# Kernel tuning notes

Hardware: AMD Instinct MI355X
Metric: run time of the kernel (lower is better)

Reference implementation:

```python
import jax, jax.numpy as jnp
import numpy as np
from jax import lax

EPS = 1e-5

def binarize(x):
    # sign forward, straight-through (identity) backward, matching torch .data-trick Binarize
    return x + lax.stop_gradient(jnp.sign(x) - x)

def conv2d(x, w, pad):
    return lax.conv_general_dilated(x, w, window_strides=(1, 1),
                                    padding=[(pad, pad), (pad, pad)],
                                    dimension_numbers=('NCHW', 'OIHW', 'NCHW'))

def maxpool_k2s1(x):
    return lax.reduce_window(x, -jnp.inf, lax.max, (1, 1, 2, 2), (1, 1, 1, 1), 'VALID')

def batchnorm(x, g, b):
    # training-mode BN: batch statistics over (N, H, W)
    mean = jnp.mean(x, axis=(0, 2, 3), keepdims=True)
    var = jnp.var(x, axis=(0, 2, 3), keepdims=True)
    return (x - mean) * lax.rsqrt(var + EPS) * g[None, :, None, None] + b[None, :, None, None]

def hardtanh(x):
    return jnp.clip(x, -1.0, 1.0)

def setup_inputs() -> dict:
    key = jax.random.key(0)
    ks = jax.random.split(key, 11)
    B = 4096
    return {
        'x':   jax.random.normal(ks[0], (B, 12, 12, 15), jnp.float32),
        'w1':  jax.random.normal(ks[1], (48, 12, 3, 3), jnp.float32) * 0.1,
        'g1':  1.0 + 0.1 * jax.random.normal(ks[2], (48,), jnp.float32),
        'b1':  0.1 * jax.random.normal(ks[3], (48,), jnp.float32),
        'w2':  jax.random.normal(ks[4], (48, 48, 3, 3), jnp.float32) * 0.1,
        'g2':  1.0 + 0.1 * jax.random.normal(ks[5], (48,), jnp.float32),
        'b2':  0.1 * jax.random.normal(ks[6], (48,), jnp.float32),
        'w3':  jax.random.normal(ks[7], (48, 48, 3, 3), jnp.float32) * 0.1,
        'g3':  1.0 + 0.1 * jax.random.normal(ks[8], (48,), jnp.float32),
        'b3':  0.1 * jax.random.normal(ks[9], (48,), jnp.float32),
        'wfc': jax.random.normal(ks[10], (5, 54 * 48), jnp.float32) * 0.02,
    }

def reference(x, w1, g1, b1, w2, g2, b2, w3, g3, b3, wfc):
    # BinarizeConv2d binarizes activations (in_channels != 3) and weights; returns binarized input too
    xb1 = binarize(x)                                  # [B,12,12,15]
    h = conv2d(xb1, binarize(w1), pad=1)               # [B,48,12,15]
    h = maxpool_k2s1(h)                                # [B,48,11,14]
    h = hardtanh(batchnorm(h, g1, b1))
    xb2 = binarize(h)
    h = conv2d(xb2, binarize(w2), pad=0)               # [B,48,9,12]
    h = hardtanh(batchnorm(h, g2, b2))
    xb3 = binarize(h)
    h = conv2d(xb3, binarize(w3), pad=0)               # [B,48,7,10]
    h = maxpool_k2s1(h)                                # [B,48,6,9] -> 54 spatial
    h = hardtanh(batchnorm(h, g3, b3))
    f = h.reshape(h.shape[0], -1)                      # [B, 2592]
    fb = binarize(f)
    out = fb @ binarize(wfc).T                         # [B, 5]  (LogSoftmax defined but never applied)
    return (out, xb1, xb2, xb3, fb)
```

## Files before the change

kernel.cpp:

```cpp
#include <hip/hip_runtime.h>
#include <stdint.h>

typedef unsigned long long u64;
typedef unsigned int u32;
typedef unsigned short u16;
typedef unsigned char u8;
typedef signed char s8;

#define NB 4096

#define WS_STATS 0
#define WS_W1Q   20480
#define WS_W2P   24576
#define WS_W3P   28672
#define WS_WFCP  32768
#define WS_A2    40960
#define WS_P1    5087232
#define WS_P3    5087232

#define OUT_OFF 0
#define XB1_OFF 20480
#define XB2_OFF 8867840
#define XB3_OFF 39145472
#define FB_OFF  60379136

__device__ __forceinline__ float fsign(float v) {
    return (v > 0.0f) ? 1.0f : ((v < 0.0f) ? -1.0f : 0.0f);
}
__device__ __forceinline__ int sh16(int v, int h) {
    return h ? (v >> 16) : (int)(short)v;
}

__global__ __launch_bounds__(512)
void kw_pack(const float* __restrict__ w1, const float* __restrict__ w2,
             const float* __restrict__ w3, const float* __restrict__ wfc,
             u32* __restrict__ W1Q, u64* __restrict__ W2P, u64* __restrict__ W3P,
             u64* __restrict__ WFCP, long long* __restrict__ stats) {
    int t = threadIdx.x;
    for (int i = t; i < 2304; i += 512) stats[i] = 0;
    if (t < 48) {
        u16 m1[9];
        #pragma unroll
        for (int p = 0; p < 9; ++p) {
            u16 m = 0;
            for (int c = 0; c < 12; ++c)
                if (w1[t*108 + c*9 + p] > 0.0f) m |= (u16)(1u << c);
            m1[p] = m;
        }
        #pragma unroll
        for (int j = 0; j < 4; ++j)
            W1Q[t*5 + j] = (u32)m1[2*j] | ((u32)m1[2*j+1] << 16);
        W1Q[t*5 + 4] = (u32)m1[8];
    }
    if (t < 432) {
        int oc = t / 9, p = t % 9;
        u64 m2 = 0, m3 = 0;
        for (int c = 0; c < 48; ++c) {
            if (w2[oc*432 + c*9 + p] > 0.0f) m2 |= (1ull << c);
            if (w3[oc*432 + c*9 + p] > 0.0f) m3 |= (1ull << c);
        }
        W2P[t] = m2;
        W3P[t] = m3;
    }
    if (t < 205) {
        int o = t / 41, j = t % 41;
        u64 m = 0;
        for (int l = 0; l < 64; ++l) {
            int k = j*64 + l;
            if (k < 2592 && wfc[o*2592 + k] > 0.0f) m |= (1ull << l);
        }
        WFCP[t] = m;
    }
}

__global__ __launch_bounds__(192)
void k1(const float* __restrict__ x, const u32* __restrict__ W1Q,
        float* __restrict__ dout, u8* __restrict__ P1g, u64* __restrict__ stats) {
    __shared__ u8 bitsb[2160];
    __shared__ u16 As[180];
    __shared__ int cmap[2304];
    __shared__ int2 part[192];
    int t = threadIdx.x, b = blockIdx.x;
    {
        const float4* xp = (const float4*)(x + (size_t)b*2160);
        float4* xo = (float4*)(dout + XB1_OFF + (size_t)b*2160);
        for (int j = t; j < 540; j += 192) {
            float4 v = xp[j];
            float4 o;
            o.x = fsign(v.x); o.y = fsign(v.y); o.z = fsign(v.z); o.w = fsign(v.w);
            xo[j] = o;
            bitsb[4*j]   = v.x > 0.0f;
            bitsb[4*j+1] = v.y > 0.0f;
            bitsb[4*j+2] = v.z > 0.0f;
            bitsb[4*j+3] = v.w > 0.0f;
        }
    }
    __syncthreads();
    if (t < 180) {
        u16 m = 0;
        #pragma unroll
        for (int c = 0; c < 12; ++c)
            m |= ((u16)bitsb[c*180 + t]) << c;
        As[t] = m;
    }
    __syncthreads();
    if (t < 180) {
        int y = t / 15, xx = t % 15;
        u16 tap[9], msk[9];
        int nv = 0;
        #pragma unroll
        for (int ky = 0; ky < 3; ++ky) {
            #pragma unroll
            for (int kx = 0; kx < 3; ++kx) {
                int yy = y + ky - 1, xc = xx + kx - 1;
                bool v = (yy >= 0 && yy < 12 && xc >= 0 && xc < 15);
                int yl = min(max(yy, 0), 11), xl = min(max(xc, 0), 14);
                tap[ky*3+kx] = As[yl*15 + xl];
                msk[ky*3+kx] = v ? (u16)0xFFFF : (u16)0;
                nv += v ? 12 : 0;
            }
        }
        u32 tq[5], mq[5];
        #pragma unroll
        for (int j = 0; j < 4; ++j) {
            tq[j] = (u32)tap[2*j] | ((u32)tap[2*j+1] << 16);
            mq[j] = (u32)msk[2*j] | ((u32)msk[2*j+1] << 16);
        }
        tq[4] = tap[8]; mq[4] = msk[8];
        s8* cb = (s8*)cmap;
        #pragma unroll 4
        for (int oc = 0; oc < 48; ++oc) {
            int acc = 0;
            #pragma unroll
            for (int j = 0; j < 5; ++j)
                acc += __popc((tq[j] ^ W1Q[oc*5 + j]) & mq[j]);
            cb[oc*192 + y*16 + xx] = (s8)(nv - 2*acc);
        }
    }
    __syncthreads();
    {
        int c = t >> 2, q = t & 3;
        int r0 = 3*q, nr = (q < 3) ? 3 : 2;
        int rowv[4][4];
        #pragma unroll
        for (int j = 0; j < 4; ++j)
            if (j <= nr) {
                #pragma unroll
                for (int i = 0; i < 4; ++i)
                    rowv[j][i] = cmap[c*48 + (r0 + j)*4 + i];
            }
        int sum = 0, sq = 0;
        u8* gp = P1g + (size_t)b*8448 + c*176;
        #pragma unroll
        for (int pr = 0; pr < 3; ++pr) {
            if (pr < nr) {
                int o0 = 0, o1 = 0, o2 = 0, o3 = 0;
                #pragma unroll
                for (int k = 0; k < 14; ++k) {
                    int a0 = (int)(s8)(rowv[pr][k>>2] >> (8*(k&3)));
                    int a1 = (int)(s8)(rowv[pr][(k+1)>>2] >> (8*((k+1)&3)));
                    int b0 = (int)(s8)(rowv[pr+1][k>>2] >> (8*(k&3)));
                    int b1 = (int)(s8)(rowv[pr+1][(k+1)>>2] >> (8*((k+1)&3)));
                    int mx = max(max(a0, a1), max(b0, b1));
                    sum += mx; sq += mx*mx;
                    int shl = 8*(k&3);
                    if ((k>>2) == 0) o0 |= (mx & 255) << shl;
                    else if ((k>>2) == 1) o1 |= (mx & 255) << shl;
                    else if ((k>>2) == 2) o2 |= (mx & 255) << shl;
                    else o3 |= (mx & 255) << shl;
                }
                *((int4*)(gp + (r0 + pr)*16)) = make_int4(o0, o1, o2, o3);
            }
        }
        part[t] = make_int2(sum, sq);
    }
    __syncthreads();
    if (t < 48) {
        int s = 0, q = 0;
        #pragma unroll
        for (int k = 0; k < 4; ++k) { s += part[t*4+k].x; q += part[t*4+k].y; }
        int slot = b & 7;
        atomicAdd(&stats[t*8 + slot],        (u64)(long long)s);
        atomicAdd(&stats[(48 + t)*8 + slot], (u64)(long long)q);
    }
}

__global__ __launch_bounds__(256)
void kA(const float* __restrict__ g1, const float* __restrict__ b1,
        const long long* __restrict__ statsIn, const u8* __restrict__ P1g,
        u64* __restrict__ A2, const u64* __restrict__ W2,
        u64* __restrict__ statsOut) {
    __shared__ float sc[48], sh[48];
    __shared__ u64 As[154];
    __shared__ short c2s[5184];
    __shared__ int2 part[192];
    int t = threadIdx.x, b = blockIdx.x;
    if (t < 48) {
        long long s = 0, q = 0;
        #pragma unroll
        for (int k = 0; k < 8; ++k) { s += statsIn[t*8 + k]; q += statsIn[(48 + t)*8 + k]; }
        double N = 630784.0;
        double mean = (double)s / N;
        double var  = (double)q / N - mean*mean;
        double scale = (double)g1[t] / sqrt(var + 1e-5);
        sc[t] = (float)scale;
        sh[t] = (float)((double)b1[t] - mean*scale);
    }
    __syncthreads();
    if (t < 154) {
        int row = t / 14, px = t - 14*row;
        const u8* pb = P1g + (size_t)b*8448 + row*16 + px;
        u64 m = 0;
        #pragma unroll
        for (int c = 0; c < 48; ++c)
            if (sc[c]*(float)(s8)pb[c*176] + sh[c] > 0.0f) m |= (1ull << c);
        As[t] = m;
        A2[(size_t)b*154 + t] = m;
    }
    __syncthreads();
    if (t < 216) {
        int pos = (t < 108) ? t : (t - 108);
        int ocb = (t < 108) ? 0 : 24;
        int oy = pos / 12, ox = pos - 12*oy;
        u64 tap[9];
        #pragma unroll
        for (int ky = 0; ky < 3; ++ky)
            #pragma unroll
            for (int kx = 0; kx < 3; ++kx)
                tap[ky*3+kx] = As[(oy+ky)*14 + ox + kx];
        #pragma unroll 4
        for (int oc = ocb; oc < ocb + 24; ++oc) {
            int acc = 0;
            #pragma unroll
            for (int k = 0; k < 9; ++k)
                acc += __popcll(tap[k] ^ W2[oc*9 + k]);
            c2s[oc*108 + pos] = (short)(432 - 2*acc);
        }
    }
    __syncthreads();
    if (t < 192) {
        int c = t >> 2, q = t & 3;
        const int* ci = (const int*)(c2s + c*108);
        int sum = 0, sq = 0;
        for (int j = q; j < 54; j += 4) {
            int v2 = ci[j];
            int lo = (int)(short)v2, hi = v2 >> 16;
            sum += lo + hi; sq += lo*lo + hi*hi;
        }
        part[t] = make_int2(sum, sq);
    }
    __syncthreads();
    if (t < 48) {
        int s = 0, q = 0;
        #pragma unroll
        for (int k = 0; k < 4; ++k) { s += part[t*4+k].x; q += part[t*4+k].y; }
        int slot = b & 7;
        atomicAdd(&statsOut[(96 + t)*8 + slot],  (u64)(long long)s);
        atomicAdd(&statsOut[(144 + t)*8 + slot], (u64)(long long)q);
    }
}

__global__ __launch_bounds__(256)
void kS2(const float* __restrict__ g1, const float* __restrict__ b1,
         const long long* __restrict__ statsIn, const u8* __restrict__ P1g,
         float* __restrict__ dout) {
    __shared__ float sc[48], sh[48];
    int t = threadIdx.x;
    if (t < 48) {
        long long s = 0, q = 0;
        #pragma unroll
        for (int k = 0; k < 8; ++k) { s += statsIn[t*8 + k]; q += statsIn[(48 + t)*8 + k]; }
        double N = 630784.0;
        double mean = (double)s / N;
        double var  = (double)q / N - mean*mean;
        double scale = (double)g1[t] / sqrt(var + 1e-5);
        sc[t] = (float)scale;
        sh[t] = (float)((double)b1[t] - mean*scale);
    }
    __syncthreads();
    float4* xo = (float4*)(dout + XB2_OFF);
    int gid = blockIdx.x*256 + t;
    for (int j = gid; j < 7569408; j += 1048576) {
        int base = 4*j;
        int b = base / 7392;
        int u = base - 7392*b;
        const u8* pb = P1g + (size_t)b*8448;
        float r[4];
        #pragma unroll
        for (int k = 0; k < 4; ++k) {
            int uk = u + k;
            int c = uk / 154;
            int s = uk - 154*c;
            int row = s / 14;
            int px = s - 14*row;
            int v = (int)(s8)pb[c*176 + row*16 + px];
            r[k] = fsign(sc[c]*(float)v + sh[c]);
        }
        float4 o; o.x = r[0]; o.y = r[1]; o.z = r[2]; o.w = r[3];
        xo[j] = o;
    }
}

__global__ __launch_bounds__(256)
void kB(const float* __restrict__ g2, const float* __restrict__ b2,
        const long long* __restrict__ statsIn, const u64* __restrict__ A2,
        const u64* __restrict__ W2, const u64* __restrict__ W3,
        float* __restrict__ dout, int* __restrict__ P3i,
        u64* __restrict__ statsOut) {
    __shared__ float sc[48], sh[48];
    __shared__ u64 As[154];
    __shared__ short c2s[5184];
    __shared__ u64 A3[108];
    __shared__ short cm[3360];
    __shared__ int2 part[192];
    int t = threadIdx.x, b = blockIdx.x;
    if (t < 154) As[t] = A2[(size_t)b*154 + t];
    if (t < 48) {
        long long s = 0, q = 0;
        #pragma unroll
        for (int k = 0; k < 8; ++k) { s += statsIn[(96 + t)*8 + k]; q += statsIn[(144 + t)*8 + k]; }
        double N = 442368.0;
        double mean = (double)s / N;
        double var  = (double)q / N - mean*mean;
        double scale = (double)g2[t] / sqrt(var + 1e-5);
        sc[t] = (float)scale;
        sh[t] = (float)((double)b2[t] - mean*scale);
    }
    __syncthreads();
    if (t < 216) {
        int pos = (t < 108) ? t : (t - 108);
        int ocb = (t < 108) ? 0 : 24;
        int oy = pos / 12, ox = pos - 12*oy;
        u64 tap[9];
        #pragma unroll
        for (int ky = 0; ky < 3; ++ky)
            #pragma unroll
            for (int kx = 0; kx < 3; ++kx)
                tap[ky*3+kx] = As[(oy+ky)*14 + ox + kx];
        #pragma unroll 4
        for (int oc = ocb; oc < ocb + 24; ++oc) {
            int acc = 0;
            #pragma unroll
            for (int k = 0; k < 9; ++k)
                acc += __popcll(tap[k] ^ W2[oc*9 + k]);
            c2s[oc*108 + pos] = (short)(432 - 2*acc);
        }
    }
    __syncthreads();
    float4* xo = (float4*)(dout + XB3_OFF + (size_t)b*5184);
    for (int i4 = t; i4 < 1296; i4 += 256) {
        int c = i4 / 27, s4 = i4 - 27*c;
        short4 v4 = *(const short4*)&c2s[c*108 + s4*4];
        float4 o;
        o.x = fsign(sc[c]*(float)v4.x + sh[c]);
        o.y = fsign(sc[c]*(float)v4.y + sh[c]);
        o.z = fsign(sc[c]*(float)v4.z + sh[c]);
        o.w = fsign(sc[c]*(float)v4.w + sh[c]);
        xo[i4] = o;
    }
    if (t < 108) {
        u64 m = 0;
        #pragma unroll
        for (int c = 0; c < 48; ++c)
            if (sc[c]*(float)c2s[c*108 + t] + sh[c] > 0.0f) m |= (1ull << c);
        A3[t] = m;
    }
    __syncthreads();
    if (t < 210) {
        int grp = (t < 70) ? 0 : ((t < 140) ? 1 : 2);
        int pos = t - grp*70;
        int ocb = grp*16;
        int oy = pos / 10, ox = pos - 10*oy;
        u64 tap[9];
        #pragma unroll
        for (int ky = 0; ky < 3; ++ky)
            #pragma unroll
            for (int kx = 0; kx < 3; ++kx)
                tap[ky*3+kx] = A3[(oy+ky)*12 + ox + kx];
        #pragma unroll 4
        for (int oc = ocb; oc < ocb + 16; ++oc) {
            int acc = 0;
            #pragma unroll
            for (int k = 0; k < 9; ++k)
                acc += __popcll(tap[k] ^ W3[oc*9 + k]);
            cm[oc*70 + pos] = (short)(432 - 2*acc);
        }
    }
    __syncthreads();
    {
        int c = t >> 2, q = t & 3;
        if (t < 192) {
            int pr0 = (q < 2) ? 2*q : (q + 2);
            int npr = (q < 2) ? 2 : 1;
            int rowv[3][5];
            const int* cmi = (const int*)(cm + c*70);
            #pragma unroll
            for (int j = 0; j < 3; ++j)
                if (j <= npr) {
                    #pragma unroll
                    for (int i = 0; i < 5; ++i)
                        rowv[j][i] = cmi[(pr0 + j)*5 + i];
                }
            int sum = 0, sq = 0;
            int* gp = P3i + (size_t)b*1440 + c*30;
            #pragma unroll
            for (int pr = 0; pr < 2; ++pr) {
                if (pr < npr) {
                    int o[5] = {0, 0, 0, 0, 0};
                    #pragma unroll
                    for (int k = 0; k < 9; ++k) {
                        int a0 = sh16(rowv[pr][k>>1], k&1);
                        int a1 = sh16(rowv[pr][(k+1)>>1], (k+1)&1);
                        int b0 = sh16(rowv[pr+1][k>>1], k&1);
                        int b1 = sh16(rowv[pr+1][(k+1)>>1], (k+1)&1);
                        int mx = max(max(a0, a1), max(b0, b1));
                        sum += mx; sq += mx*mx;
                        o[k>>1] |= (mx & 0xffff) << (16*(k&1));
                    }
                    #pragma unroll
                    for (int j = 0; j < 5; ++j) gp[(pr0 + pr)*5 + j] = o[j];
                }
            }
            part[t] = make_int2(sum, sq);
        }
    }
    __syncthreads();
    if (t < 48) {
        int s = 0, q = 0;
        #pragma unroll
        for (int k = 0; k < 4; ++k) { s += part[t*4+k].x; q += part[t*4+k].y; }
        int slot = b & 7;
        atomicAdd(&statsOut[(192 + t)*8 + slot], (u64)(long long)s);
        atomicAdd(&statsOut[(240 + t)*8 + slot], (u64)(long long)q);
    }
}

__global__ __launch_bounds__(256)
void kC(const float* __restrict__ g3, const float* __restrict__ b3,
        const long long* __restrict__ statsIn, const int4* __restrict__ P3g4,
        const u64* __restrict__ WFC, float* __restrict__ dout) {
    __shared__ float sc[48], sh[48];
    __shared__ int smP[1440];
    __shared__ u8 nib[648];
    __shared__ u64 fbb[41];
    int t = threadIdx.x, b = blockIdx.x;
    for (int i = t; i < 360; i += 256) ((int4*)smP)[i] = P3g4[(size_t)b*360 + i];
    if (t < 48) {
        long long s = 0, q = 0;
        #pragma unroll
        for (int k = 0; k < 8; ++k) { s += statsIn[(192 + t)*8 + k]; q += statsIn[(240 + t)*8 + k]; }
        double N = 221184.0;
        double mean = (double)s / N;
        double var  = (double)q / N - mean*mean;
        double scale = (double)g3[t] / sqrt(var + 1e-5);
        sc[t] = (float)scale;
        sh[t] = (float)((double)b3[t] - mean*scale);
    }
    __syncthreads();
    const short* smS = (const short*)smP;
    float4* fo = (float4*)(dout + FB_OFF + (size_t)b*2592);
    for (int i4 = t; i4 < 648; i4 += 256) {
        int i = 4*i4;
        float r[4];
        unsigned n = 0;
        #pragma unroll
        for (int k = 0; k < 4; ++k) {
            int idx = i + k;
            int c = idx / 54, s = idx - 54*c;
            int row = s / 9, px = s - 9*row;
            float bn = sc[c]*(float)smS[c*60 + row*10 + px] + sh[c];
            r[k] = fsign(bn);
            if (bn > 0.0f) n |= (1u << k);
        }
        float4 o; o.x = r[0]; o.y = r[1]; o.z = r[2]; o.w = r[3];
        fo[i4] = o;
        nib[i4] = (u8)n;
    }
    __syncthreads();
    if (t < 41) {
        u64 m = 0;
        #pragma unroll
        for (int k = 0; k < 16; ++k) {
            int j = t*16 + k;
            if (j < 648) m |= ((u64)nib[j]) << (4*k);
        }
        fbb[t] = m;
    }
    __syncthreads();
    if (t < 5) {
        const u64* Wf = WFC + t*41;
        int acc = 0;
        #pragma unroll
        for (int j = 0; j < 41; ++j) acc += __popcll(fbb[j] ^ Wf[j]);
        dout[OUT_OFF + b*5 + t] = (float)(2592 - 2*acc);
    }
}

extern "C" void kernel_launch(void* const* d_in, const int* in_sizes, int n_in,
                              void* d_out, int out_size, void* d_ws, size_t ws_size,
                              hipStream_t stream) {
    const float* x   = (const float*)d_in[0];
    const float* w1  = (const float*)d_in[1];
    const float* g1  = (const float*)d_in[2];
    const float* b1  = (const float*)d_in[3];
    const float* w2  = (const float*)d_in[4];
    const float* g2  = (const float*)d_in[5];
    const float* b2  = (const float*)d_in[6];
    const float* w3  = (const float*)d_in[7];
    const float* g3  = (const float*)d_in[8];
    const float* b3  = (const float*)d_in[9];
    const float* wfc = (const float*)d_in[10];
    float* out = (float*)d_out;
    char* ws = (char*)d_ws;

    long long* stats = (long long*)(ws + WS_STATS);
    u32*       W1Q   = (u32*)(ws + WS_W1Q);
    u64*       W2P   = (u64*)(ws + WS_W2P);
    u64*       W3P   = (u64*)(ws + WS_W3P);
    u64*       WFCP  = (u64*)(ws + WS_WFCP);
    u64*       A2    = (u64*)(ws + WS_A2);
    u8*        P1g   = (u8*)(ws + WS_P1);
    int*       P3i   = (int*)(ws + WS_P3);

    hipLaunchKernelGGL(kw_pack, dim3(1),    dim3(512), 0, stream,
                       w1, w2, w3, wfc, W1Q, W2P, W3P, WFCP, stats);
    hipLaunchKernelGGL(k1,      dim3(NB),   dim3(192), 0, stream,
                       x, W1Q, out, P1g, (u64*)stats);
    hipLaunchKernelGGL(kA,      dim3(NB),   dim3(256), 0, stream,
                       g1, b1, stats, P1g, A2, W2P, (u64*)stats);
    hipLaunchKernelGGL(kS2,     dim3(NB),   dim3(256), 0, stream,
                       g1, b1, stats, P1g, out);
    hipLaunchKernelGGL(kB,      dim3(NB),   dim3(256), 0, stream,
                       g2, b2, stats, A2, W2P, W3P, out, P3i, (u64*)stats);
    hipLaunchKernelGGL(kC,      dim3(NB),   dim3(256), 0, stream,
                       g3, b3, stats, (const int4*)P3i, WFCP, out);
}
```

Measured before the change: 641.9 us.

## Split fused per-image BNN pipeline into many flat element-parallel kernels

Replaces the per-image fused kernels kA, kB and kC with a chain of small flat kernels. These finalize the BN constants once, pack activations, run conv2 without recomputing it, reduce per-channel stats, and handle conv3 with fused maxpool, the fb output and an FC step done by wavefront ballot. Conv2 was previously computed twice (once in kA for stats and again in kB); it is now computed once and stored channel-major in global memory. The cost is extra global round trips for the intermediate tensors, more kernel launches, and single-block-per-channel stat reductions with only 48 blocks, which limits parallelism.

```diff
diff --git a/kernel.cpp b/kernel.cpp
--- a/kernel.cpp
+++ b/kernel.cpp
@@ -10,13 +10,17 @@
 #define NB 4096
 
 #define WS_STATS 0
+#define WS_CST   18432
 #define WS_W1Q   20480
 #define WS_W2P   24576
 #define WS_W3P   28672
 #define WS_WFCP  32768
 #define WS_A2    40960
 #define WS_P1    5087232
-#define WS_P3    5087232
+#define WS_C2T   5087232
+#define WS_P3T   5087232
+#define WS_P3B   26320896
+#define WS_A3    40960
 
 #define OUT_OFF 0
 #define XB1_OFF 20480
@@ -70,6 +74,23 @@
             if (k < 2592 && wfc[o*2592 + k] > 0.0f) m |= (1ull << l);
         }
         WFCP[t] = m;
+    }
+}
+
+__global__ __launch_bounds__(64)
+void kbn(const float* __restrict__ g, const float* __restrict__ bb,
+         const long long* __restrict__ st, float* __restrict__ cst, float Nf) {
+    int t = threadIdx.x;
+    if (t < 48) {
+        long long s = 0, q = 0;
+        #pragma unroll
+        for (int k = 0; k < 8; ++k) { s += st[t*8 + k]; q += st[(48 + t)*8 + k]; }
+        double N = (double)Nf;
+        double mean = (double)s / N;
+        double var  = (double)q / N - mean*mean;
+        double scale = (double)g[t] / sqrt(var + 1e-5);
+        cst[t]      = (float)scale;
+        cst[48 + t] = (float)((double)bb[t] - mean*scale);
     }
 }
 
@@ -186,97 +207,31 @@
 }
 
 __global__ __launch_bounds__(256)
-void kA(const float* __restrict__ g1, const float* __restrict__ b1,
-        const long long* __restrict__ statsIn, const u8* __restrict__ P1g,
-        u64* __restrict__ A2, const u64* __restrict__ W2,
-        u64* __restrict__ statsOut) {
+void kM2(const float* __restrict__ cst, const u8* __restrict__ P1g,
+         u64* __restrict__ A2) {
     __shared__ float sc[48], sh[48];
-    __shared__ u64 As[154];
-    __shared__ short c2s[5184];
-    __shared__ int2 part[192];
-    int t = threadIdx.x, b = blockIdx.x;
-    if (t < 48) {
-        long long s = 0, q = 0;
-        #pragma unroll
-        for (int k = 0; k < 8; ++k) { s += statsIn[t*8 + k]; q += statsIn[(48 + t)*8 + k]; }
-        double N = 630784.0;
-        double mean = (double)s / N;
-        double var  = (double)q / N - mean*mean;
-        double scale = (double)g1[t] / sqrt(var + 1e-5);
-        sc[t] = (float)scale;
-        sh[t] = (float)((double)b1[t] - mean*scale);
-    }
-    __syncthreads();
-    if (t < 154) {
-        int row = t / 14, px = t - 14*row;
-        const u8* pb = P1g + (size_t)b*8448 + row*16 + px;
-        u64 m = 0;
-        #pragma unroll
-        for (int c = 0; c < 48; ++c)
-            if (sc[c]*(float)(s8)pb[c*176] + sh[c] > 0.0f) m |= (1ull << c);
-        As[t] = m;
-        A2[(size_t)b*154 + t] = m;
-    }
-    __syncthreads();
-    if (t < 216) {
-        int pos = (t < 108) ? t : (t - 108);
-        int ocb = (t < 108) ? 0 : 24;
-        int oy = pos / 12, ox = pos - 12*oy;
-        u64 tap[9];
-        #pragma unroll
-        for (int ky = 0; ky < 3; ++ky)
-            #pragma unroll
-            for (int kx = 0; kx < 3; ++kx)
-                tap[ky*3+kx] = As[(oy+ky)*14 + ox + kx];
-        #pragma unroll 4
-        for (int oc = ocb; oc < ocb + 24; ++oc) {
-            int acc = 0;
-            #pragma unroll
-            for (int k = 0; k < 9; ++k)
-                acc += __popcll(tap[k] ^ W2[oc*9 + k]);
-            c2s[oc*108 + pos] = (short)(432 - 2*acc);
-        }
-    }
-    __syncthreads();
-    if (t < 192) {
-        int c = t >> 2, q = t & 3;
-        const int* ci = (const int*)(c2s + c*108);
-        int sum = 0, sq = 0;
-        for (int j = q; j < 54; j += 4) {
-            int v2 = ci[j];
-            int lo = (int)(short)v2, hi = v2 >> 16;
-            sum += lo + hi; sq += lo*lo + hi*hi;
-        }
-        part[t] = make_int2(sum, sq);
-    }
-    __syncthreads();
-    if (t < 48) {
-        int s = 0, q = 0;
-        #pragma unroll
-        for (int k = 0; k < 4; ++k) { s += part[t*4+k].x; q += part[t*4+k].y; }
-        int slot = b & 7;
-        atomicAdd(&statsOut[(96 + t)*8 + slot],  (u64)(long long)s);
-        atomicAdd(&statsOut[(144 + t)*8 + slot], (u64)(long long)q);
-    }
-}
-
-__global__ __launch_bounds__(256)
-void kS2(const float* __restrict__ g1, const float* __restrict__ b1,
-         const long long* __restrict__ statsIn, const u8* __restrict__ P1g,
+    int t = threadIdx.x;
+    if (t < 48) sc[t] = cst[t];
+    else if (t < 96) sh[t-48] = cst[t];
+    __syncthreads();
+    int g = blockIdx.x*256 + t;
+    int b = g / 154, s = g - 154*b;
+    int row = s / 14, px = s - 14*row;
+    const u8* pb = P1g + (size_t)b*8448 + row*16 + px;
+    u64 m = 0;
+    #pragma unroll
+    for (int c = 0; c < 48; ++c)
+        if (sc[c]*(float)(s8)pb[c*176] + sh[c] > 0.0f) m |= (1ull << c);
+    A2[g] = m;
+}
+
+__global__ __launch_bounds__(256)
+void kS2(const float* __restrict__ cst, const u8* __restrict__ P1g,
          float* __restrict__ dout) {
     __shared__ float sc[48], sh[48];
     int t = threadIdx.x;
-    if (t < 48) {
-        long long s = 0, q = 0;
-        #pragma unroll
-        for (int k = 0; k < 8; ++k) { s += statsIn[t*8 + k]; q += statsIn[(48 + t)*8 + k]; }
-        double N = 630784.0;
-        double mean = (double)s / N;
-        double var  = (double)q / N - mean*mean;
-        double scale = (double)g1[t] / sqrt(var + 1e-5);
-        sc[t] = (float)scale;
-        sh[t] = (float)((double)b1[t] - mean*scale);
-    }
+    if (t < 48) sc[t] = cst[t];
+    else if (t < 96) sh[t-48] = cst[t];
     __syncthreads();
     float4* xo = (float4*)(dout + XB2_OFF);
     int gid = blockIdx.x*256 + t;
@@ -302,197 +257,211 @@
 }
 
 __global__ __launch_bounds__(256)
-void kB(const float* __restrict__ g2, const float* __restrict__ b2,
-        const long long* __restrict__ statsIn, const u64* __restrict__ A2,
-        const u64* __restrict__ W2, const u64* __restrict__ W3,
-        float* __restrict__ dout, int* __restrict__ P3i,
-        u64* __restrict__ statsOut) {
+void kCv2(const u64* __restrict__ A2, const u64* __restrict__ W2,
+          short* __restrict__ C2T) {
+    __shared__ u64 W2s[432];
+    int t = threadIdx.x;
+    for (int i = t; i < 432; i += 256) W2s[i] = W2[i];
+    __syncthreads();
+    int g = blockIdx.x*256 + t;
+    int b = g / 108, s = g - 108*b;
+    int oy = s / 12, ox = s - 12*oy;
+    const u64* ab = A2 + (size_t)b*154;
+    u64 tap[9];
+    #pragma unroll
+    for (int ky = 0; ky < 3; ++ky)
+        #pragma unroll
+        for (int kx = 0; kx < 3; ++kx)
+            tap[ky*3+kx] = ab[(oy+ky)*14 + ox + kx];
+    #pragma unroll 4
+    for (int oc = 0; oc < 48; ++oc) {
+        int acc = 0;
+        #pragma unroll
+        for (int k = 0; k < 9; ++k)
+            acc += __popcll(tap[k] ^ W2s[oc*9 + k]);
+        C2T[(size_t)oc*442368 + b*108 + s] = (short)(432 - 2*acc);
+    }
+}
+
+__global__ __launch_bounds__(256)
+void kSt(const short* __restrict__ src, int perChan,
+         long long* __restrict__ stats, int base) {
+    __shared__ long long redS[4], redQ[4];
+    int t = threadIdx.x, c = blockIdx.x;
+    const int* p = (const int*)(src + (size_t)c*perChan);
+    int n2 = perChan >> 1;
+    int sum = 0, sq = 0;
+    for (int j = t; j < n2; j += 256) {
+        int v2 = p[j];
+        int lo = (int)(short)v2, hi = v2 >> 16;
+        sum += lo + hi; sq += lo*lo + hi*hi;
+    }
+    long long ls = sum, lq = sq;
+    #pragma unroll
+    for (int off = 32; off >= 1; off >>= 1) {
+        ls += __shfl_down(ls, off);
+        lq += __shfl_down(lq, off);
+    }
+    int wv = t >> 6, ln = t & 63;
+    if (ln == 0) { redS[wv] = ls; redQ[wv] = lq; }
+    __syncthreads();
+    if (t == 0) {
+        long long S = redS[0]+redS[1]+redS[2]+redS[3];
+        long long Q = redQ[0]+redQ[1]+redQ[2]+redQ[3];
+        stats[(base + c)*8]      = S;
+        stats[(base + 48 + c)*8] = Q;
+    }
+}
+
+__global__ __launch_bounds__(256)
+void kX3(const float* __restrict__ cst, const short* __restrict__ C2T,
+         float* __restrict__ dout) {
     __shared__ float sc[48], sh[48];
-    __shared__ u64 As[154];
-    __shared__ short c2s[5184];
-    __shared__ u64 A3[108];
-    __shared__ short cm[3360];
-    __shared__ int2 part[192];
-    int t = threadIdx.x, b = blockIdx.x;
-    if (t < 154) As[t] = A2[(size_t)b*154 + t];
-    if (t < 48) {
-        long long s = 0, q = 0;
-        #pragma unroll
-        for (int k = 0; k < 8; ++k) { s += statsIn[(96 + t)*8 + k]; q += statsIn[(144 + t)*8 + k]; }
-        double N = 442368.0;
-        double mean = (double)s / N;
-        double var  = (double)q / N - mean*mean;
-        double scale = (double)g2[t] / sqrt(var + 1e-5);
-        sc[t] = (float)scale;
-        sh[t] = (float)((double)b2[t] - mean*scale);
-    }
-    __syncthreads();
-    if (t < 216) {
-        int pos = (t < 108) ? t : (t - 108);
-        int ocb = (t < 108) ? 0 : 24;
-        int oy = pos / 12, ox = pos - 12*oy;
-        u64 tap[9];
-        #pragma unroll
-        for (int ky = 0; ky < 3; ++ky)
+    int t = threadIdx.x;
+    if (t < 48) sc[t] = cst[t];
+    else if (t < 96) sh[t-48] = cst[t];
+    __syncthreads();
+    int g = blockIdx.x*256 + t;
+    int b = g / 1296, i4 = g - 1296*b;
+    int c = i4 / 27, s4 = i4 - 27*c;
+    const short* p = C2T + (size_t)c*442368 + b*108 + s4*4;
+    short4 v4 = *(const short4*)p;
+    float4 o;
+    o.x = fsign(sc[c]*(float)v4.x + sh[c]);
+    o.y = fsign(sc[c]*(float)v4.y + sh[c]);
+    o.z = fsign(sc[c]*(float)v4.z + sh[c]);
+    o.w = fsign(sc[c]*(float)v4.w + sh[c]);
+    ((float4*)(dout + XB3_OFF))[(size_t)b*1296 + i4] = o;
+}
+
+__global__ __launch_bounds__(256)
+void kM3(const float* __restrict__ cst, const short* __restrict__ C2T,
+         u64* __restrict__ A3) {
+    __shared__ float sc[48], sh[48];
+    int t = threadIdx.x;
+    if (t < 48) sc[t] = cst[t];
+    else if (t < 96) sh[t-48] = cst[t];
+    __syncthreads();
+    int g = blockIdx.x*256 + t;
+    int b = g / 108, s = g - 108*b;
+    u64 m = 0;
+    #pragma unroll
+    for (int c = 0; c < 48; ++c) {
+        short v = C2T[(size_t)c*442368 + b*108 + s];
+        if (sc[c]*(float)v + sh[c] > 0.0f) m |= (1ull << c);
+    }
+    A3[g] = m;
+}
+
+__global__ __launch_bounds__(256)
+void kCv3P(const u64* __restrict__ A3, const u64* __restrict__ W3,
+           short* __restrict__ P3T, short* __restrict__ P3B) {
+    __shared__ u64 W3s[432];
+    int t = threadIdx.x;
+    for (int i = t; i < 432; i += 256) W3s[i] = W3[i];
+    __syncthreads();
+    int g = blockIdx.x*256 + t;
+    int b = g / 108, r = g - 108*b;
+    int grp = r / 54, s = r - 54*grp;
+    int ocb = grp*24;
+    int py = s / 9, px = s - 9*py;
+    const u64* ab = A3 + (size_t)b*108;
+    u64 tp[4][4];
+    #pragma unroll
+    for (int j = 0; j < 4; ++j)
+        #pragma unroll
+        for (int i = 0; i < 4; ++i)
+            tp[j][i] = ab[(py+j)*12 + px + i];
+    for (int oc = ocb; oc < ocb + 24; ++oc) {
+        int rs[4][2];
+        #pragma unroll
+        for (int j = 0; j < 4; ++j) {
             #pragma unroll
-            for (int kx = 0; kx < 3; ++kx)
-                tap[ky*3+kx] = As[(oy+ky)*14 + ox + kx];
-        #pragma unroll 4
-        for (int oc = ocb; oc < ocb + 24; ++oc) {
-            int acc = 0;
+            for (int sx = 0; sx < 2; ++sx) {
+                int a = 0;
+                #pragma unroll
+                for (int kx = 0; kx < 3; ++kx)
+                    a += __popcll(tp[j][kx+sx] ^ W3s[oc*9 + 0*3 + kx]);
+                rs[j][sx] = a;
+            }
+        }
+        int c00, c01, c10, c11;
+        {
+            int a00=0,a01=0,a10=0,a11=0;
             #pragma unroll
-            for (int k = 0; k < 9; ++k)
-                acc += __popcll(tap[k] ^ W2[oc*9 + k]);
-            c2s[oc*108 + pos] = (short)(432 - 2*acc);
-        }
-    }
-    __syncthreads();
-    float4* xo = (float4*)(dout + XB3_OFF + (size_t)b*5184);
-    for (int i4 = t; i4 < 1296; i4 += 256) {
-        int c = i4 / 27, s4 = i4 - 27*c;
-        short4 v4 = *(const short4*)&c2s[c*108 + s4*4];
-        float4 o;
-        o.x = fsign(sc[c]*(float)v4.x + sh[c]);
-        o.y = fsign(sc[c]*(float)v4.y + sh[c]);
-        o.z = fsign(sc[c]*(float)v4.z + sh[c]);
-        o.w = fsign(sc[c]*(float)v4.w + sh[c]);
-        xo[i4] = o;
-    }
-    if (t < 108) {
-        u64 m = 0;
-        #pragma unroll
-        for (int c = 0; c < 48; ++c)
-            if (sc[c]*(float)c2s[c*108 + t] + sh[c] > 0.0f) m |= (1ull << c);
-        A3[t] = m;
-    }
-    __syncthreads();
-    if (t < 210) {
-        int grp = (t < 70) ? 0 : ((t < 140) ? 1 : 2);
-        int pos = t - grp*70;
-        int ocb = grp*16;
-        int oy = pos / 10, ox = pos - 10*oy;
-        u64 tap[9];
-        #pragma unroll
-        for (int ky = 0; ky < 3; ++ky)
-            #pragma unroll
-            for (int kx = 0; kx < 3; ++kx)
-                tap[ky*3+kx] = A3[(oy+ky)*12 + ox + kx];
-        #pragma unroll 4
-        for (int oc = ocb; oc < ocb + 16; ++oc) {
-            int acc = 0;
-            #pragma unroll
-            for (int k = 0; k < 9; ++k)
-                acc += __popcll(tap[k] ^ W3[oc*9 + k]);
-            cm[oc*70 + pos] = (short)(432 - 2*acc);
-        }
-    }
-    __syncthreads();
-    {
-        int c = t >> 2, q = t & 3;
-        if (t < 192) {
-            int pr0 = (q < 2) ? 2*q : (q + 2);
-            int npr = (q < 2) ? 2 : 1;
-            int rowv[3][5];
-            const int* cmi = (const int*)(cm + c*70);
-            #pragma unroll
-            for (int j = 0; j < 3; ++j)
-                if (j <= npr) {
-                    #pragma unroll
-                    for (int i = 0; i < 5; ++i)
-                        rowv[j][i] = cmi[(pr0 + j)*5 + i];
-                }
-            int sum = 0, sq = 0;
-            int* gp = P3i + (size_t)b*1440 + c*30;
-            #pragma unroll
-            for (int pr = 0; pr < 2; ++pr) {
-                if (pr < npr) {
-                    int o[5] = {0, 0, 0, 0, 0};
-                    #pragma unroll
-                    for (int k = 0; k < 9; ++k) {
-                        int a0 = sh16(rowv[pr][k>>1], k&1);
-                        int a1 = sh16(rowv[pr][(k+1)>>1], (k+1)&1);
-                        int b0 = sh16(rowv[pr+1][k>>1], k&1);
-                        int b1 = sh16(rowv[pr+1][(k+1)>>1], (k+1)&1);
-                        int mx = max(max(a0, a1), max(b0, b1));
-                        sum += mx; sq += mx*mx;
-                        o[k>>1] |= (mx & 0xffff) << (16*(k&1));
-                    }
-                    #pragma unroll
-                    for (int j = 0; j < 5; ++j) gp[(pr0 + pr)*5 + j] = o[j];
+            for (int ky = 0; ky < 3; ++ky) {
+                #pragma unroll
+                for (int kx = 0; kx < 3; ++kx) {
+                    u64 w = W3s[oc*9 + ky*3 + kx];
+                    a00 += __popcll(tp[ky][kx]     ^ w);
+                    a01 += __popcll(tp[ky][kx+1]   ^ w);
+                    a10 += __popcll(tp[ky+1][kx]   ^ w);
+                    a11 += __popcll(tp[ky+1][kx+1] ^ w);
                 }
             }
-            part[t] = make_int2(sum, sq);
-        }
-    }
-    __syncthreads();
-    if (t < 48) {
-        int s = 0, q = 0;
-        #pragma unroll
-        for (int k = 0; k < 4; ++k) { s += part[t*4+k].x; q += part[t*4+k].y; }
-        int slot = b & 7;
-        atomicAdd(&statsOut[(192 + t)*8 + slot], (u64)(long long)s);
-        atomicAdd(&statsOut[(240 + t)*8 + slot], (u64)(long long)q);
-    }
-}
-
-__global__ __launch_bounds__(256)
-void kC(const float* __restrict__ g3, const float* __restrict__ b3,
-        const long long* __restrict__ statsIn, const int4* __restrict__ P3g4,
-        const u64* __restrict__ WFC, float* __restrict__ dout) {
+            c00 = 432 - 2*a00; c01 = 432 - 2*a01;
+            c10 = 432 - 2*a10; c11 = 432 - 2*a11;
+        }
+        (void)rs;
+        int mx = max(max(c00, c01), max(c10, c11));
+        P3T[(size_t)oc*221184 + b*54 + s] = (short)mx;
+        P3B[(size_t)b*2592 + oc*54 + s]   = (short)mx;
+    }
+}
+
+__global__ __launch_bounds__(256)
+void kFB(const float* __restrict__ cst, const short* __restrict__ P3B,
+         float* __restrict__ dout) {
     __shared__ float sc[48], sh[48];
-    __shared__ int smP[1440];
-    __shared__ u8 nib[648];
-    __shared__ u64 fbb[41];
-    int t = threadIdx.x, b = blockIdx.x;
-    for (int i = t; i < 360; i += 256) ((int4*)smP)[i] = P3g4[(size_t)b*360 + i];
-    if (t < 48) {
-        long long s = 0, q = 0;
-        #pragma unroll
-        for (int k = 0; k < 8; ++k) { s += statsIn[(192 + t)*8 + k]; q += statsIn[(240 + t)*8 + k]; }
-        double N = 221184.0;
-        double mean = (double)s / N;
-        double var  = (double)q / N - mean*mean;
-        double scale = (double)g3[t] / sqrt(var + 1e-5);
-        sc[t] = (float)scale;
-        sh[t] = (float)((double)b3[t] - mean*scale);
-    }
-    __syncthreads();
-    const short* smS = (const short*)smP;
-    float4* fo = (float4*)(dout + FB_OFF + (size_t)b*2592);
-    for (int i4 = t; i4 < 648; i4 += 256) {
-        int i = 4*i4;
-        float r[4];
-        unsigned n = 0;
-        #pragma unroll
-        for (int k = 0; k < 4; ++k) {
-            int idx = i + k;
-            int c = idx / 54, s = idx - 54*c;
-            int row = s / 9, px = s - 9*row;
-            float bn = sc[c]*(float)smS[c*60 + row*10 + px] + sh[c];
-            r[k] = fsign(bn);
-            if (bn > 0.0f) n |= (1u << k);
-        }
-        float4 o; o.x = r[0]; o.y = r[1]; o.z = r[2]; o.w = r[3];
-        fo[i4] = o;
-        nib[i4] = (u8)n;
-    }
-    __syncthreads();
-    if (t < 41) {
-        u64 m = 0;
-        #pragma unroll
-        for (int k = 0; k < 16; ++k) {
-            int j = t*16 + k;
-            if (j < 648) m |= ((u64)nib[j]) << (4*k);
-        }
-        fbb[t] = m;
-    }
-    __syncthreads();
-    if (t < 5) {
-        const u64* Wf = WFC + t*41;
-        int acc = 0;
-        #pragma unroll
-        for (int j = 0; j < 41; ++j) acc += __popcll(fbb[j] ^ Wf[j]);
-        dout[OUT_OFF + b*5 + t] = (float)(2592 - 2*acc);
+    int t = threadIdx.x;
+    if (t < 48) sc[t] = cst[t];
+    else if (t < 96) sh[t-48] = cst[t];
+    __syncthreads();
+    int g = blockIdx.x*256 + t;
+    int b = g / 648, i4 = g - 648*b;
+    int idx = 4*i4;
+    const short* p = P3B + (size_t)b*2592 + idx;
+    short4 v4 = *(const short4*)p;
+    int c0 = idx/54, c1 = (idx+1)/54, c2 = (idx+2)/54, c3 = (idx+3)/54;
+    float4 o;
+    o.x = fsign(sc[c0]*(float)v4.x + sh[c0]);
+    o.y = fsign(sc[c1]*(float)v4.y + sh[c1]);
+    o.z = fsign(sc[c2]*(float)v4.z + sh[c2]);
+    o.w = fsign(sc[c3]*(float)v4.w + sh[c3]);
+    ((float4*)(dout + FB_OFF))[(size_t)b*648 + i4] = o;
+}
+
+__global__ __launch_bounds__(256)
+void kFC(const float* __restrict__ cst, const short* __restrict__ P3B,
+         const u64* __restrict__ WFC, float* __restrict__ dout) {
+    __shared__ float sc[48], sh[48];
+    __shared__ u64 WFCs[205];
+    int t = threadIdx.x;
+    if (t < 48) sc[t] = cst[t];
+    else if (t < 96) sh[t-48] = cst[t];
+    if (t < 205) WFCs[t] = WFC[t];
+    __syncthreads();
+    int wv = t >> 6, ln = t & 63;
+    int b = blockIdx.x*4 + wv;
+    const short* p = P3B + (size_t)b*2592;
+    u64 myword = 0;
+    for (int w = 0; w < 41; ++w) {
+        int k = w*64 + ln;
+        bool pred = false;
+        if (k < 2592) {
+            int c = k / 54;
+            pred = sc[c]*(float)p[k] + sh[c] > 0.0f;
+        }
+        u64 ball = __ballot(pred);
+        if (ln == w) myword = ball;
+    }
+    #pragma unroll
+    for (int o = 0; o < 5; ++o) {
+        long long contrib = (ln < 41) ? (long long)__popcll(myword ^ WFCs[o*41 + ln]) : 0;
+        #pragma unroll
+        for (int off = 32; off >= 1; off >>= 1)
+            contrib += __shfl_down(contrib, off);
+        if (ln == 0) dout[OUT_OFF + b*5 + o] = (float)(2592 - 2*(int)contrib);
     }
 }
 
@@ -514,24 +483,43 @@
     char* ws = (char*)d_ws;
 
     long long* stats = (long long*)(ws + WS_STATS);
+    float*     cst   = (float*)(ws + WS_CST);
     u32*       W1Q   = (u32*)(ws + WS_W1Q);
     u64*       W2P   = (u64*)(ws + WS_W2P);
     u64*       W3P   = (u64*)(ws + WS_W3P);
     u64*       WFCP  = (u64*)(ws + WS_WFCP);
     u64*       A2    = (u64*)(ws + WS_A2);
+    u64*       A3    = (u64*)(ws + WS_A3);
     u8*        P1g   = (u8*)(ws + WS_P1);
-    int*       P3i   = (int*)(ws + WS_P3);
-
-    hipLaunchKernelGGL(kw_pack, dim3(1),    dim3(512), 0, stream,
+    short*     C2T   = (short*)(ws + WS_C2T);
+    short*     P3T   = (short*)(ws + WS_P3T);
+    short*     P3B   = (short*)(ws + WS_P3B);
+
+    hipLaunchKernelGGL(kw_pack, dim3(1),     dim3(512), 0, stream,
                        w1, w2, w3, wfc, W1Q, W2P, W3P, WFCP, stats);
-    hipLaunchKernelGGL(k1,      dim3(NB),   dim3(192), 0, stream,
+    hipLaunchKernelGGL(k1,      dim3(NB),    dim3(192), 0, stream,
                        x, W1Q, out, P1g, (u64*)stats);
-    hipLaunchKernelGGL(kA,      dim3(NB),   dim3(256), 0, stream,
-                       g1, b1, stats, P1g, A2, W2P, (u64*)stats);
-    hipLaunchKernelGGL(kS2,     dim3(NB),   dim3(256), 0, stream,
-                       g1, b1, stats, P1g, out);
-    hipLaunchKernelGGL(kB,      dim3(NB),   dim3(256), 0, stream,
-                       g2, b2, stats, A2, W2P, W3P, out, P3i, (u64*)stats);
-    hipLaunchKernelGGL(kC,      dim3(NB),   dim3(256), 0, stream,
-                       g3, b3, stats, (const int4*)P3i, WFCP, out);
-}
+    hipLaunchKernelGGL(kbn,     dim3(1),     dim3(64),  0, stream,
+                       g1, b1, stats, cst, 630784.0f);
+    hipLaunchKernelGGL(kM2,     dim3(2464),  dim3(256), 0, stream, cst, P1g, A2);
+    hipLaunchKernelGGL(kS2,     dim3(4096),  dim3(256), 0, stream, cst, P1g, out);
+    hipLaunchKernelGGL(kCv2,    dim3(1728),  dim3(256), 0, stream, A2, W2P, C2T);
+    hipLaunchKernelGGL(kSt,     dim3(48),    dim3(256), 0, stream,
+                       C2T, 442368, stats, 96);
+    hipLaunchKernelGGL(kbn,     dim3(1),     dim3(64),  0, stream,
+                       g2, b2, stats + 96*8, cst + 96, 442368.0f);
+    hipLaunchKernelGGL(kX3,     dim3(20736), dim3(256), 0, stream,
+                       cst + 96, C2T, out);
+    hipLaunchKernelGGL(kM3,     dim3(1728),  dim3(256), 0, stream,
+                       cst + 96, C2T, A3);
+    hipLaunchKernelGGL(kCv3P,   dim3(1728),  dim3(256), 0, stream,
+                       A3, W3P, P3T, P3B);
+    hipLaunchKernelGGL(kSt,     dim3(48),    dim3(256), 0, stream,
+                       P3T, 221184, stats, 192);
+    hipLaunchKernelGGL(kbn,     dim3(1),     dim3(64),  0, stream,
+                       g3, b3, stats + 192*8, cst + 192, 221184.0f);
+    hipLaunchKernelGGL(kFB,     dim3(10368), dim3(256), 0, stream,
+                       cst + 192, P3B, out);
+    hipLaunchKernelGGL(kFC,     dim3(1024),  dim3(256), 0, stream,
+                       cst + 192, P3B, WFCP, out);
+}
```

New measurement: 767.6 us. 1.2x slower.
